# Performance work log

Hardware: AMD Instinct MI355X
Metric: run time of the kernel (lower is better)

## Reference

```python
import jax, jax.numpy as jnp
import numpy as np
from jax import lax

KH, KW = 3, 3
CIN, F = 32, 32
WSIZE = KH * KW * CIN * F  # 9216


def setup_inputs() -> dict:
    key = jax.random.key(0)
    k1, k2 = jax.random.split(key)
    x = jax.random.normal(k1, (32, 128, 128, CIN), dtype=jnp.float32)
    # hypernetwork output: per-sample flattened kernel (+ bias)
    params = jax.random.normal(k2, (32, WSIZE + F), dtype=jnp.float32) * 0.05
    return {"x": x, "params": params}


def reference(x, params):
    B = x.shape[0]
    # kernel_shape = (kh, kw, input_dim, filters) per keras channels_last
    W = params[:, :WSIZE].reshape(B, KH, KW, CIN, F)  # [B, kh, kw, Cin, F]
    b = params[:, WSIZE:]                              # [B, F]

    def conv_one(xi, wi, bi):
        # xi: [H, W, Cin], wi: [kh, kw, Cin, F] (HWIO), bi: [F]
        out = lax.conv_general_dilated(
            xi[None], wi,
            window_strides=(1, 1), padding="SAME",
            dimension_numbers=("NHWC", "HWIO", "NHWC"),
        )
        return out[0] + bi  # broadcast bias over H, W

    # per-sample dynamic convolution, vectorized over batch
    return jax.vmap(conv_one)(x, W, b)  # activation=None -> linear
```

## Files before the change

kernel.cpp:

```cpp
#include <hip/hip_runtime.h>


typedef __attribute__((ext_vector_type(8))) short bf16x8;
typedef __attribute__((ext_vector_type(4))) float f32x4;

constexpr int HWD  = 128, CINC = 32, FC = 32;
constexpr int WSZ  = 9 * CINC * FC;
constexpr int PSTR = WSZ + FC;

constexpr int XS_PLANE  = 4 * 130 * 16;
constexpr int XS_BYTES  = 4 * (XS_PLANE + 32);
constexpr int WT_BYTES  = 36 * 32 * 16;

constexpr size_t WS_FRAGS = 32ull * 36 * 32;
constexpr size_t WS_NEED  = WS_FRAGS * 16;

__device__ __forceinline__ int xs_off(int cig, int r, int col) {
    return ((cig * 4 + r) * 130 + col) * 16 + cig * 32;
}
__device__ __forceinline__ int wt_off(int kgrp, int f) {
    return XS_BYTES + (kgrp * 32 + f) * 16;
}

__device__ __forceinline__ unsigned short f2bf(float f) {
    unsigned u = __float_as_uint(f);
    return (unsigned short)((u + 0x7FFFu + ((u >> 16) & 1u)) >> 16);
}
__device__ __forceinline__ bf16x8 pack8(float4 a, float4 b) {
    bf16x8 r;
    r[0] = (short)f2bf(a.x); r[1] = (short)f2bf(a.y);
    r[2] = (short)f2bf(a.z); r[3] = (short)f2bf(a.w);
    r[4] = (short)f2bf(b.x); r[5] = (short)f2bf(b.y);
    r[6] = (short)f2bf(b.z); r[7] = (short)f2bf(b.w);
    return r;
}

__global__ __launch_bounds__(256) void wprep(
    const float* __restrict__ params, bf16x8* __restrict__ ws)
{
    const int b   = blockIdx.y;
    const int seg = blockIdx.x;
    const float* __restrict__ pw = params + (size_t)b * PSTR;
    #pragma unroll
    for (int i = 0; i < 2; ++i) {
        const int idx = threadIdx.x + i * 256;
        if (idx < 288) {
            const int c  = seg * 288 + idx;
            const int sg = c >> 5;
            const int f  = c & 31;
            const float* p = pw + (size_t)(sg * 8) * FC + f;
            float4 a, bb;
            a.x  = p[0 * FC]; a.y  = p[1 * FC]; a.z  = p[2 * FC]; a.w  = p[3 * FC];
            bb.x = p[4 * FC]; bb.y = p[5 * FC]; bb.z = p[6 * FC]; bb.w = p[7 * FC];
            ws[(size_t)b * 1152 + c] = pack8(a, bb);
        }
    }
}

template<bool USE_WS>
__global__ __launch_bounds__(256, USE_WS ? 4 : 3) void conv3x3_mfma(
    const float* __restrict__ x, const float* __restrict__ params,
    float* __restrict__ out, const bf16x8* __restrict__ ws)
{
    __shared__ __align__(16) unsigned char smem[XS_BYTES + (USE_WS ? 0 : WT_BYTES)];

    const int hw      = blockIdx.x;
    const int logical = (hw & 7) * 256 + (hw >> 3);
    const int b       = logical >> 6;
    const int y0      = (logical & 63) * 2;

    const int t = threadIdx.x;
    const float* __restrict__ xb = x + (size_t)b * (HWD * HWD * CINC);
    const float* __restrict__ pw = params + (size_t)b * PSTR;

    #pragma unroll
    for (int i = 0; i < 9; ++i) {
        const int c = t + i * 256;
        if (c < 2080) {
            const int cig      = c & 3;
            const unsigned q   = (unsigned)(c >> 2);
            const unsigned r   = q / 130u;
            const unsigned col = q - r * 130u;
            const int iy   = y0 - 1 + (int)r;
            const int icol = (int)col - 1;
            bf16x8 v = 0;
            if ((unsigned)iy < 128u && (unsigned)icol < 128u) {
                const float* p = xb + ((size_t)iy * HWD + icol) * CINC + cig * 8;
                v = pack8(*(const float4*)(p), *(const float4*)(p + 4));
            }
            *(bf16x8*)(smem + xs_off(cig, (int)r, (int)col)) = v;
        }
    }

    if constexpr (!USE_WS) {
        #pragma unroll
        for (int j = 0; j < 5; ++j) {
            const int c    = t + j * 256;
            const int kgrp = c >> 5;
            const int f    = c & 31;
            if (kgrp < 36) {
                const float* p = pw + (size_t)(kgrp * 8) * FC + f;
                float4 a, bb;
                a.x  = p[0 * FC]; a.y  = p[1 * FC]; a.z  = p[2 * FC]; a.w  = p[3 * FC];
                bb.x = p[4 * FC]; bb.y = p[5 * FC]; bb.z = p[6 * FC]; bb.w = p[7 * FC];
                *(bf16x8*)(smem + wt_off(kgrp, f)) = pack8(a, bb);
            }
        }
    }
    __syncthreads();

    const int wv   = t >> 6;
    const int ln   = t & 63;
    const int lg   = ln >> 4;
    const int li   = ln & 15;
    const int yloc = wv >> 1;
    const int xw   = (wv & 1) * 64;

    f32x4 acc[4][2];
    #pragma unroll
    for (int i = 0; i < 4; ++i) { acc[i][0] = (f32x4)0.0f; acc[i][1] = (f32x4)0.0f; }

    const size_t wsb = (size_t)b * 1152 + lg * 32;

    bf16x8 bc0, bc1;
    if constexpr (USE_WS) {
        bc0 = ws[wsb + li];
        bc1 = ws[wsb + 16 + li];
    }

    #pragma unroll
    for (int s = 0; s < 9; ++s) {
        const int kh = s / 3, kw = s % 3;
        bf16x8 b0, b1, bn0, bn1;
        if constexpr (USE_WS) {
            if (s < 8) {
                bn0 = ws[wsb + (s + 1) * 128 + li];
                bn1 = ws[wsb + (s + 1) * 128 + 16 + li];
            }
            b0 = bc0; b1 = bc1;
        } else {
            b0 = *(const bf16x8*)(smem + wt_off(s * 4 + lg, li));
            b1 = *(const bf16x8*)(smem + wt_off(s * 4 + lg, 16 + li));
        }
        const int r = yloc + kh;
        const int colbase = xw + li + kw;
        #pragma unroll
        for (int tI = 0; tI < 4; ++tI) {
            const bf16x8 a = *(const bf16x8*)(smem + xs_off(lg, r, colbase + tI * 16));
            acc[tI][0] = __builtin_amdgcn_mfma_f32_16x16x32_bf16(a, b0, acc[tI][0], 0, 0, 0);
            acc[tI][1] = __builtin_amdgcn_mfma_f32_16x16x32_bf16(a, b1, acc[tI][1], 0, 0, 0);
        }
        if constexpr (USE_WS) { bc0 = bn0; bc1 = bn1; }
    }

    const float bias0 = pw[WSZ + li];
    const float bias1 = pw[WSZ + 16 + li];
    const int yo = y0 + yloc;
    float* __restrict__ ob = out + ((size_t)(b * HWD + yo)) * (HWD * FC);

    #pragma unroll
    for (int tI = 0; tI < 4; ++tI) {
        #pragma unroll
        for (int reg = 0; reg < 4; ++reg) {
            const int px = xw + tI * 16 + lg * 4 + reg;
            float* q = ob + (size_t)px * FC;
            q[li]      = acc[tI][0][reg] + bias0;
            q[16 + li] = acc[tI][1][reg] + bias1;
        }
    }
}

extern "C" void kernel_launch(void* const* d_in, const int* in_sizes, int n_in,
                              void* d_out, int out_size, void* d_ws, size_t ws_size,
                              hipStream_t stream)
{
    const float* x      = (const float*)d_in[0];
    const float* params = (const float*)d_in[1];
    float*       out    = (float*)d_out;

    if (ws_size >= WS_NEED && d_ws != nullptr) {
        bf16x8* ws = (bf16x8*)d_ws;
        hipLaunchKernelGGL(wprep, dim3(4, 32), dim3(256), 0, stream, params, ws);
        hipLaunchKernelGGL((conv3x3_mfma<true>), dim3(2048), dim3(256), 0, stream,
                           x, params, out, (const bf16x8*)ws);
    } else {
        hipLaunchKernelGGL((conv3x3_mfma<false>), dim3(2048), dim3(256), 0, stream,
                           x, params, out, (const bf16x8*)nullptr);
    }
}
```

Before: 127.1 us.

## Batch global loads before packing, swap MFMA operands for vectorized float4 stores

Issues all input-tile global loads into registers up front and packs them to bf16 afterwards, so the loads can be in flight together. The weight prefetch is also moved ahead of the staging loop. MFMA operands are swapped so each lane holds four consecutive filters for one pixel, which allows float4 output stores and a float4 bias load. The pack now uses a cheaper perm-based rounding that is not ties-to-even. This raises register pressure (18 float4 per thread held live), which may reduce occupancy under the launch bounds.

Result: slower. 130.4 us (+2.6%).

```diff
diff --git a/kernel.cpp b/kernel.cpp
--- a/kernel.cpp
+++ b/kernel.cpp
@@ -33,6 +33,20 @@
     r[4] = (short)f2bf(b.x); r[5] = (short)f2bf(b.y);
     r[6] = (short)f2bf(b.z); r[7] = (short)f2bf(b.w);
     return r;
+}
+
+__device__ __forceinline__ unsigned pk2(float lo, float hi) {
+    const unsigned a = __float_as_uint(lo) + 0x8000u;
+    const unsigned b = __float_as_uint(hi) + 0x8000u;
+    return __builtin_amdgcn_perm(b, a, 0x07060302u);
+}
+__device__ __forceinline__ bf16x8 pack8f(float4 a, float4 b) {
+    union { int4 i; bf16x8 h; } u;
+    u.i.x = (int)pk2(a.x, a.y);
+    u.i.y = (int)pk2(a.z, a.w);
+    u.i.z = (int)pk2(b.x, b.y);
+    u.i.w = (int)pk2(b.z, b.w);
+    return u.h;
 }
 
 __global__ __launch_bounds__(256) void wprep(
@@ -73,6 +87,40 @@
     const float* __restrict__ xb = x + (size_t)b * (HWD * HWD * CINC);
     const float* __restrict__ pw = params + (size_t)b * PSTR;
 
+    const int wv   = t >> 6;
+    const int ln   = t & 63;
+    const int lg   = ln >> 4;
+    const int li   = ln & 15;
+    const int yloc = wv >> 1;
+    const int xw   = (wv & 1) * 64;
+
+    const size_t wsb = (size_t)b * 1152 + lg * 32;
+
+    float4 xr[9][2];
+    bool   inr[9];
+    #pragma unroll
+    for (int i = 0; i < 9; ++i) {
+        const int c = t + i * 256;
+        const int cig      = c & 3;
+        const unsigned q   = (unsigned)(c >> 2);
+        const unsigned r   = q / 130u;
+        const unsigned col = q - r * 130u;
+        const int iy   = y0 - 1 + (int)r;
+        const int icol = (int)col - 1;
+        inr[i] = (c < 2080) && ((unsigned)iy < 128u) && ((unsigned)icol < 128u);
+        if (inr[i]) {
+            const float* p = xb + ((size_t)iy * HWD + icol) * CINC + cig * 8;
+            xr[i][0] = *(const float4*)(p);
+            xr[i][1] = *(const float4*)(p + 4);
+        }
+    }
+
+    bf16x8 bc0, bc1;
+    if constexpr (USE_WS) {
+        bc0 = ws[wsb + li];
+        bc1 = ws[wsb + 16 + li];
+    }
+
     #pragma unroll
     for (int i = 0; i < 9; ++i) {
         const int c = t + i * 256;
@@ -81,13 +129,8 @@
             const unsigned q   = (unsigned)(c >> 2);
             const unsigned r   = q / 130u;
             const unsigned col = q - r * 130u;
-            const int iy   = y0 - 1 + (int)r;
-            const int icol = (int)col - 1;
             bf16x8 v = 0;
-            if ((unsigned)iy < 128u && (unsigned)icol < 128u) {
-                const float* p = xb + ((size_t)iy * HWD + icol) * CINC + cig * 8;
-                v = pack8(*(const float4*)(p), *(const float4*)(p + 4));
-            }
+            if (inr[i]) v = pack8f(xr[i][0], xr[i][1]);
             *(bf16x8*)(smem + xs_off(cig, (int)r, (int)col)) = v;
         }
     }
@@ -109,24 +152,9 @@
     }
     __syncthreads();
 
-    const int wv   = t >> 6;
-    const int ln   = t & 63;
-    const int lg   = ln >> 4;
-    const int li   = ln & 15;
-    const int yloc = wv >> 1;
-    const int xw   = (wv & 1) * 64;
-
     f32x4 acc[4][2];
     #pragma unroll
     for (int i = 0; i < 4; ++i) { acc[i][0] = (f32x4)0.0f; acc[i][1] = (f32x4)0.0f; }
-
-    const size_t wsb = (size_t)b * 1152 + lg * 32;
-
-    bf16x8 bc0, bc1;
-    if constexpr (USE_WS) {
-        bc0 = ws[wsb + li];
-        bc1 = ws[wsb + 16 + li];
-    }
 
     #pragma unroll
     for (int s = 0; s < 9; ++s) {
@@ -147,26 +175,28 @@
         #pragma unroll
         for (int tI = 0; tI < 4; ++tI) {
             const bf16x8 a = *(const bf16x8*)(smem + xs_off(lg, r, colbase + tI * 16));
-            acc[tI][0] = __builtin_amdgcn_mfma_f32_16x16x32_bf16(a, b0, acc[tI][0], 0, 0, 0);
-            acc[tI][1] = __builtin_amdgcn_mfma_f32_16x16x32_bf16(a, b1, acc[tI][1], 0, 0, 0);
+            acc[tI][0] = __builtin_amdgcn_mfma_f32_16x16x32_bf16(b0, a, acc[tI][0], 0, 0, 0);
+            acc[tI][1] = __builtin_amdgcn_mfma_f32_16x16x32_bf16(b1, a, acc[tI][1], 0, 0, 0);
         }
         if constexpr (USE_WS) { bc0 = bn0; bc1 = bn1; }
     }
 
-    const float bias0 = pw[WSZ + li];
-    const float bias1 = pw[WSZ + 16 + li];
+    const float4 bias0 = *(const float4*)(pw + WSZ + lg * 4);
+    const float4 bias1 = *(const float4*)(pw + WSZ + 16 + lg * 4);
     const int yo = y0 + yloc;
     float* __restrict__ ob = out + ((size_t)(b * HWD + yo)) * (HWD * FC);
 
     #pragma unroll
     for (int tI = 0; tI < 4; ++tI) {
-        #pragma unroll
-        for (int reg = 0; reg < 4; ++reg) {
-            const int px = xw + tI * 16 + lg * 4 + reg;
-            float* q = ob + (size_t)px * FC;
-            q[li]      = acc[tI][0][reg] + bias0;
-            q[16 + li] = acc[tI][1][reg] + bias1;
-        }
+        const int px = xw + tI * 16 + li;
+        float* q = ob + (size_t)px * FC + lg * 4;
+        float4 v0, v1;
+        v0.x = acc[tI][0][0] + bias0.x; v0.y = acc[tI][0][1] + bias0.y;
+        v0.z = acc[tI][0][2] + bias0.z; v0.w = acc[tI][0][3] + bias0.w;
+        v1.x = acc[tI][1][0] + bias1.x; v1.y = acc[tI][1][1] + bias1.y;
+        v1.z = acc[tI][1][2] + bias1.z; v1.w = acc[tI][1][3] + bias1.w;
+        *(float4*)(q)      = v0;
+        *(float4*)(q + 16) = v1;
     }
 }
 
```
